# Kernel optimization log

Measured on AMD Instinct MI355X. Metric: run time of the kernel, lower is better.

## Reference

```python
import jax, jax.numpy as jnp
import numpy as np

N = 100000   # nodes per graph (50k users + 50k items)
E = 1600000  # edges per graph
D = 128      # feature / hidden dim
B = 100000   # train pairs per domain
NUM_USER = 50000
LAMBDA = 1.0


def setup_inputs() -> dict:
    key = jax.random.key(0)
    ks = jax.random.split(key, 24)
    s = 1.0 / np.sqrt(D)
    return {
        "feats_s": jax.random.normal(ks[0], (N, D), jnp.float32),
        "feats_t": jax.random.normal(ks[1], (N, D), jnp.float32),
        "W1": jax.random.normal(ks[2], (D, D), jnp.float32) * s,
        "b1": jnp.zeros((D,), jnp.float32),
        "W2": jax.random.normal(ks[3], (D, D), jnp.float32) * s,
        "b2": jnp.zeros((D,), jnp.float32),
        "cls_W": jax.random.normal(ks[4], (2 * D, 1), jnp.float32) * s,
        "cls_b": jnp.zeros((1,), jnp.float32),
        "du_W": jax.random.normal(ks[5], (D, 1), jnp.float32) * s,
        "du_b": jnp.zeros((1,), jnp.float32),
        "di_W": jax.random.normal(ks[6], (D, 1), jnp.float32) * s,
        "di_b": jnp.zeros((1,), jnp.float32),
        "edge_src_s": jax.random.randint(ks[7], (E,), 0, N, jnp.int32),
        "edge_dst_s": jax.random.randint(ks[8], (E,), 0, N, jnp.int32),
        "edge_src_t": jax.random.randint(ks[9], (E,), 0, N, jnp.int32),
        "edge_dst_t": jax.random.randint(ks[10], (E,), 0, N, jnp.int32),
        "user_s": jax.random.randint(ks[11], (B,), 0, NUM_USER, jnp.int32),
        "item_s": jax.random.randint(ks[12], (B,), 0, NUM_USER, jnp.int32),
        "labels_s": jax.random.randint(ks[13], (B,), 0, 2, jnp.int32),
        "user_t": jax.random.randint(ks[14], (B,), 0, NUM_USER, jnp.int32),
        "item_t": jax.random.randint(ks[15], (B,), 0, NUM_USER, jnp.int32),
        "labels_t": jax.random.randint(ks[16], (B,), 0, 2, jnp.int32),
        "num_user_ds": NUM_USER,
        "num_user_dt": NUM_USER,
    }


def _gcn_layer(x, W, b, src, dst, dinv):
    # PyG GCNConv: out[i] = sum_{j->i} dinv[j]*dinv[i] * (x @ W)[j] + b
    h = x @ W
    norm = (dinv[src] * dinv[dst])[:, None]
    return jax.ops.segment_sum(h[src] * norm, dst, num_segments=x.shape[0]) + b


def _encode(x, src, dst, W1, b1, W2, b2):
    n = x.shape[0]
    sl = jnp.arange(n, dtype=src.dtype)            # self loops
    src = jnp.concatenate([src, sl])
    dst = jnp.concatenate([dst, sl])
    deg = jax.ops.segment_sum(jnp.ones_like(dst, dtype=x.dtype), dst, num_segments=n)
    dinv = jax.lax.rsqrt(jnp.maximum(deg, 1.0))    # deg >= 1 due to self loops
    h = jax.nn.relu(_gcn_layer(x, W1, b1, src, dst, dinv))
    return _gcn_layer(h, W2, b2, src, dst, dinv)   # dropout is identity at eval


def _bce_from_logits(z, y):
    # mean BCE on sigmoid(z), numerically stable
    return jnp.mean(y * jax.nn.softplus(-z) + (1.0 - y) * jax.nn.softplus(z))


def reference(feats_s, feats_t, W1, b1, W2, b2, cls_W, cls_b, du_W, du_b, di_W, di_b,
              edge_src_s, edge_dst_s, edge_src_t, edge_dst_t,
              user_s, item_s, labels_s, user_t, item_t, labels_t,
              num_user_ds, num_user_dt):
    x_ds = _encode(feats_s, edge_src_s, edge_dst_s, W1, b1, W2, b2)
    x_dt = _encode(feats_t, edge_src_t, edge_dst_t, W1, b1, W2, b2)

    ufs = x_ds[user_s]
    ifs = x_ds[item_s + num_user_ds]
    uft = x_dt[user_t]
    ift = x_dt[item_t + num_user_dt]

    z_s = (jnp.concatenate([ufs, ifs], axis=1) @ cls_W).reshape(-1) + cls_b[0]
    z_t = (jnp.concatenate([uft, ift], axis=1) @ cls_W).reshape(-1) + cls_b[0]
    clf_loss = _bce_from_logits(z_s, labels_s.astype(jnp.float32)) + \
               _bce_from_logits(z_t, labels_t.astype(jnp.float32))

    cu_s = jax.nn.sigmoid((ufs @ du_W).reshape(-1) + du_b[0])
    cu_t = jax.nn.sigmoid((uft @ du_W).reshape(-1) + du_b[0])
    ci_s = jax.nn.sigmoid((ifs @ di_W).reshape(-1) + di_b[0])
    ci_t = jax.nn.sigmoid((ift @ di_W).reshape(-1) + di_b[0])
    domain_loss = jnp.abs(jnp.mean(cu_s) - jnp.mean(cu_t)) + \
                  jnp.abs(jnp.mean(ci_s) - jnp.mean(ci_t))

    return clf_loss + LAMBDA * domain_loss
```

## Files before the change

### kernel.cpp

```cpp
#include <hip/hip_runtime.h>

#define D 128
#define NB 512
#define BSLACK 4160
#define CHUNK 8

typedef __attribute__((ext_vector_type(8))) short bf16x8;
typedef __attribute__((ext_vector_type(4))) float f32x4;
typedef __attribute__((ext_vector_type(2))) float f32x2;
typedef __attribute__((ext_vector_type(4))) int i32x4;

static __device__ inline unsigned pack_bf16x2(float a, float b) {
    unsigned ua = __float_as_uint(a);
    unsigned ub = __float_as_uint(b);
    ua += 0x7fffu + ((ua >> 16) & 1u);
    ub += 0x7fffu + ((ub >> 16) & 1u);
    return (ua >> 16) | (ub & 0xffff0000u);
}

__global__ __launch_bounds__(256) void bh_k(const int* __restrict__ dst_s,
                                            const int* __restrict__ dst_t,
                                            int* __restrict__ bcnt, int E) {
    int d = blockIdx.y;
    const int* dst = d ? dst_t : dst_s;
    __shared__ int h[NB];
    for (int i = threadIdx.x; i < NB; i += 256) h[i] = 0;
    __syncthreads();
    int stride = gridDim.x * 256;
    for (int e = blockIdx.x * 256 + threadIdx.x; e < E; e += stride)
        atomicAdd(&h[dst[e] >> 8], 1);
    __syncthreads();
    for (int i = threadIdx.x; i < NB; i += 256)
        if (h[i]) atomicAdd(&bcnt[d * NB + i], h[i]);
}

__global__ __launch_bounds__(1024) void scanB_k(const int* __restrict__ bcnt,
                                                int* __restrict__ bbase,
                                                int* __restrict__ cursor) {
    __shared__ int sh[1024];
    int t = threadIdx.x;
    int v = bcnt[t];
    sh[t] = v;
    __syncthreads();
    for (int o = 1; o < 1024; o <<= 1) {
        int x = (t >= o) ? sh[t - o] : 0;
        __syncthreads();
        sh[t] += x;
        __syncthreads();
    }
    int ex = sh[t] - v;
    bbase[t] = ex; cursor[t] = ex;
    if (t == 1023) bbase[1024] = sh[1023];
}

__global__ __launch_bounds__(256) void bin_k(const int* __restrict__ src_s,
                                             const int* __restrict__ dst_s,
                                             const int* __restrict__ src_t,
                                             const int* __restrict__ dst_t,
                                             int* __restrict__ cursor,
                                             unsigned* __restrict__ pairs, int E) {
    int d = blockIdx.y;
    const int* src = d ? src_t : src_s;
    const int* dst = d ? dst_t : dst_s;
    int* cur = cursor + d * NB;
    __shared__ int h[NB];
    __shared__ int gb[NB];
    int t0 = blockIdx.x * 2048;
    if (t0 >= E) return;
    for (int i = threadIdx.x; i < NB; i += 256) h[i] = 0;
    __syncthreads();
    int rank[8]; unsigned pk[8]; short bk[8];
    #pragma unroll
    for (int j = 0; j < 8; ++j) {
        int e = t0 + j * 256 + threadIdx.x;
        if (e < E) {
            int dd = dst[e], s = src[e];
            bk[j] = (short)(dd >> 8);
            pk[j] = (unsigned)s | ((unsigned)(dd & 255) << 24);
            rank[j] = atomicAdd(&h[dd >> 8], 1);
        } else bk[j] = -1;
    }
    __syncthreads();
    for (int i = threadIdx.x; i < NB; i += 256)
        gb[i] = h[i] ? atomicAdd(&cur[i], h[i]) : 0;
    __syncthreads();
    #pragma unroll
    for (int j = 0; j < 8; ++j)
        if (bk[j] >= 0) pairs[gb[bk[j]] + rank[j]] = pk[j];
}

__global__ __launch_bounds__(256) void csrb_k(const unsigned* __restrict__ pairs,
                                              const int* __restrict__ bbase,
                                              int2* __restrict__ nspan,
                                              float* __restrict__ dinv,
                                              int* __restrict__ csr, int N) {
    int d = blockIdx.y, bx = blockIdx.x, t = threadIdx.x;
    int g = d * NB + bx;
    int e0 = bbase[g], e1 = bbase[g + 1];
    int cbase = ((e0 + 15) & ~15) + g * BSLACK;
    float* dv = dinv + (size_t)d * (N + 1);
    int2* ns = nspan + (size_t)d * N;
    __shared__ int lh[256];
    __shared__ int lex[256];
    __shared__ int lc[256];
    lh[t] = 0; lc[t] = 0;
    __syncthreads();
    for (int e = e0 + t; e < e1; e += 256)
        atomicAdd(&lh[pairs[e] >> 24], 1);
    __syncthreads();
    int node = (bx << 8) + t;
    bool valid = node < N;
    int deg = lh[t];
    int pdeg = valid ? (((deg + 16) >> 4) << 4) : 0;
    lex[t] = pdeg;
    __syncthreads();
    for (int o = 1; o < 256; o <<= 1) {
        int x = (t >= o) ? lex[t - o] : 0;
        __syncthreads();
        lex[t] += x;
        __syncthreads();
    }
    int start = cbase + lex[t] - pdeg;
    if (valid) {
        ns[node] = make_int2(start, start + pdeg);
        dv[node] = rsqrtf((float)(deg + 1));
    }
    lex[t] = start;
    __syncthreads();
    for (int e = e0 + t; e < e1; e += 256) {
        unsigned p = pairs[e];
        int dn = p >> 24;
        int rank = atomicAdd(&lc[dn], 1);
        csr[lex[dn] + rank] = (int)(p & 0xffffffu);
    }
    __syncthreads();
    if (valid) {
        int b = lex[t];
        csr[b + deg] = node;
        for (int k = deg + 1; k < pdeg; ++k) csr[b + k] = N;
    }
    if (t == 255) {
        int bend = start + pdeg;
        #pragma unroll
        for (int i = 0; i < 16; ++i) csr[bend + i] = N;
    }
    if (bx == 0 && t == 0) dv[N] = 0.f;
}

__global__ __launch_bounds__(256) void packW_k(const float* __restrict__ W1,
                                               const float* __restrict__ W2,
                                               unsigned short* __restrict__ wp1,
                                               unsigned short* __restrict__ wp2) {
    const float* W = blockIdx.x ? W2 : W1;
    unsigned short* wp = blockIdx.x ? wp2 : wp1;
    for (int idx = threadIdx.x; idx < 2048; idx += 256) {
        int f = idx >> 6, lane = idx & 63;
        int t = f >> 2, c = f & 3;
        int q = lane >> 4, nn = lane & 15;
        #pragma unroll
        for (int j = 0; j < 8; ++j) {
            unsigned u = __float_as_uint(W[(c * 32 + q * 8 + j) * 128 + t * 16 + nn]);
            u += 0x7fffu + ((u >> 16) & 1u);
            wp[idx * 8 + j] = (unsigned short)(u >> 16);
        }
    }
}

__global__ __launch_bounds__(256) void gemm_mfma(const void* __restrict__ xs,
                                                 const void* __restrict__ xt,
                                                 const unsigned short* __restrict__ wp,
                                                 unsigned* __restrict__ hb,
                                                 const float* __restrict__ dinv,
                                                 int N, int in_bf16) {
    int d = blockIdx.y;
    const void* xin = d ? xt : xs;
    unsigned* out = hb + (size_t)d * (N + 1) * 32;
    const float* dv = dinv + (size_t)d * (N + 1);
    __shared__ float cs[64 * 132];
    int tid = threadIdx.x;
    int wave = tid >> 6, lane = tid & 63;
    int quad = lane >> 4, nn = lane & 15;
    long long blockbase = (long long)blockIdx.x * 64;
    long long ar = blockbase + wave * 16 + nn;
    if (ar > N - 1) ar = N - 1;

    bf16x8 a[4];
    if (in_bf16) {
        const uint4* xr = (const uint4*)((const unsigned short*)xin + ar * 128);
        #pragma unroll
        for (int c = 0; c < 4; ++c) {
            union { uint4 u; bf16x8 v; } cv;
            cv.u = xr[c * 4 + quad];
            a[c] = cv.v;
        }
    } else {
        const float4* xr = (const float4*)((const float*)xin + ar * 128);
        #pragma unroll
        for (int c = 0; c < 4; ++c) {
            float4 lo = xr[c * 8 + quad * 2];
            float4 hi = xr[c * 8 + quad * 2 + 1];
            union { bf16x8 v; unsigned u[4]; } au;
            au.u[0] = pack_bf16x2(lo.x, lo.y);
            au.u[1] = pack_bf16x2(lo.z, lo.w);
            au.u[2] = pack_bf16x2(hi.x, hi.y);
            au.u[3] = pack_bf16x2(hi.z, hi.w);
            a[c] = au.v;
        }
    }

    f32x4 acc[8];
    #pragma unroll
    for (int t = 0; t < 8; ++t) acc[t] = (f32x4){0.f, 0.f, 0.f, 0.f};
    const bf16x8* wf = (const bf16x8*)wp;
    #pragma unroll
    for (int t = 0; t < 8; ++t) {
        #pragma unroll
        for (int c = 0; c < 4; ++c) {
            bf16x8 b = wf[(t * 4 + c) * 64 + lane];
            acc[t] = __builtin_amdgcn_mfma_f32_16x16x32_bf16(a[c], b, acc[t], 0, 0, 0);
        }
    }

    #pragma unroll
    for (int t = 0; t < 8; ++t) {
        #pragma unroll
        for (int r = 0; r < 4; ++r)
            cs[(wave * 16 + quad * 4 + r) * 132 + t * 16 + nn] = acc[t][r];
    }
    __syncthreads();

    #pragma unroll
    for (int i = 0; i < 8; ++i) {
        int idx = tid + i * 256;
        int r = idx >> 5, c4 = idx & 31;
        long long row = blockbase + r;
        if (row <= N) {
            float s = dv[row];
            const float4 v = *(const float4*)&cs[r * 132 + c4 * 4];
            int pk = __builtin_amdgcn_cvt_pk_fp8_f32(v.x * s, v.y * s, 0, false);
            pk = __builtin_amdgcn_cvt_pk_fp8_f32(v.z * s, v.w * s, pk, true);
            out[row * 32 + c4] = (unsigned)pk;
        }
    }
}

#define NTLD(p) __builtin_nontemporal_load((const i32x4*)(p))

#define AGG_GATHER(u, q0, q1)                                                \
        u[0] = hsl[(unsigned)q0.x << 5];                                     \
        u[1] = hsl[(unsigned)q0.y << 5];                                     \
        u[2] = hsl[(unsigned)q0.z << 5];                                     \
        u[3] = hsl[(unsigned)q0.w << 5];                                     \
        u[4] = hsl[(unsigned)q1.x << 5];                                     \
        u[5] = hsl[(unsigned)q1.y << 5];                                     \
        u[6] = hsl[(unsigned)q1.z << 5];                                     \
        u[7] = hsl[(unsigned)q1.w << 5];

#define AGG_CONSUME(u)                                                       \
        { f32x2 lo, hi;                                                      \
          lo = __builtin_amdgcn_cvt_pk_f32_fp8((int)u[0], false);            \
          hi = __builtin_amdgcn_cvt_pk_f32_fp8((int)u[0], true);             \
          s01 += lo; s23 += hi;                                              \
          lo = __builtin_amdgcn_cvt_pk_f32_fp8((int)u[1], false);            \
          hi = __builtin_amdgcn_cvt_pk_f32_fp8((int)u[1], true);             \
          s01 += lo; s23 += hi;                                              \
          lo = __builtin_amdgcn_cvt_pk_f32_fp8((int)u[2], false);            \
          hi = __builtin_amdgcn_cvt_pk_f32_fp8((int)u[2], true);             \
          s01 += lo; s23 += hi;                                              \
          lo = __builtin_amdgcn_cvt_pk_f32_fp8((int)u[3], false);            \
          hi = __builtin_amdgcn_cvt_pk_f32_fp8((int)u[3], true);             \
          s01 += lo; s23 += hi;                                              \
          lo = __builtin_amdgcn_cvt_pk_f32_fp8((int)u[4], false);            \
          hi = __builtin_amdgcn_cvt_pk_f32_fp8((int)u[4], true);             \
          s01 += lo; s23 += hi;                                              \
          lo = __builtin_amdgcn_cvt_pk_f32_fp8((int)u[5], false);            \
          hi = __builtin_amdgcn_cvt_pk_f32_fp8((int)u[5], true);             \
          s01 += lo; s23 += hi;                                              \
          lo = __builtin_amdgcn_cvt_pk_f32_fp8((int)u[6], false);            \
          hi = __builtin_amdgcn_cvt_pk_f32_fp8((int)u[6], true);             \
          s01 += lo; s23 += hi;                                              \
          lo = __builtin_amdgcn_cvt_pk_f32_fp8((int)u[7], false);            \
          hi = __builtin_amdgcn_cvt_pk_f32_fp8((int)u[7], true);             \
          s01 += lo; s23 += hi; }

__global__ __launch_bounds__(256) void agg1_k(const unsigned* __restrict__ hb,
                                              const float* __restrict__ dinv,
                                              const int2* __restrict__ nspan,
                                              const int* __restrict__ csr,
                                              const float* __restrict__ bias,
                                              uint2* __restrict__ abuf, int N) {
    int d = blockIdx.y;
    const unsigned* hs = hb + (size_t)d * (N + 1) * 32;
    const float* dv = dinv + (size_t)d * (N + 1);
    const int2* ns = nspan + (size_t)d * N;
    uint2* out = abuf + (size_t)d * N * 32;
    int wave = threadIdx.x >> 6, lane = threadIdx.x & 63;
    int node0 = (blockIdx.x * 4 + wave) * CHUNK;
    if (node0 >= N) return;
    int cnt = min(CHUNK, N - node0);
    int half = lane >> 5, li = lane & 31;
    int lc = lane & (CHUNK - 1);
    int2 myns = make_int2(0, 0);
    float mydv = 0.f;
    if (lc < cnt) { myns = ns[node0 + lc]; mydv = dv[node0 + lc]; }
    float4 b4 = ((const float4*)bias)[li];
    const unsigned* hsl = hs + li;
    const int* cp = csr + 8 * half;

    f32x2 s01 = (f32x2){0.f, 0.f};
    f32x2 s23 = (f32x2){0.f, 0.f};

    auto finalize = [&](int k) {
        float a0 = s01[0], a1 = s01[1], a2 = s23[0], a3 = s23[1];
        a0 += __shfl_xor(a0, 32);
        a1 += __shfl_xor(a1, 32);
        a2 += __shfl_xor(a2, 32);
        a3 += __shfl_xor(a3, 32);
        float dik = __shfl(mydv, k);
        float o0 = fmaxf(fmaf(dik, a0, b4.x), 0.f);
        float o1 = fmaxf(fmaf(dik, a1, b4.y), 0.f);
        float o2 = fmaxf(fmaf(dik, a2, b4.z), 0.f);
        float o3 = fmaxf(fmaf(dik, a3, b4.w), 0.f);
        if (half == 0)
            out[(size_t)(node0 + k) * 32 + li] =
                make_uint2(pack_bf16x2(o0, o1), pack_bf16x2(o2, o3));
    };

    int k = 0;
    int e = __shfl(myns.x, 0);
    int end = __shfl(myns.y, 0);
    i32x4 c0 = NTLD(cp + e), c1 = NTLD(cp + e + 4);
    unsigned uA[8], uB[8];
    AGG_GATHER(uA, c0, c1)
    c0 = NTLD(cp + e + 16); c1 = NTLD(cp + e + 20);
    for (;;) {
        int en = e + 16;
        AGG_GATHER(uB, c0, c1)
        c0 = NTLD(cp + en + 16); c1 = NTLD(cp + en + 20);
        AGG_CONSUME(uA)
        if (en >= end) {
            finalize(k);
            if (++k >= cnt) break;
            end = __shfl(myns.y, k);
            s01 = (f32x2){0.f, 0.f};
            s23 = (f32x2){0.f, 0.f};
        }
        e = en;
        en = e + 16;
        AGG_GATHER(uA, c0, c1)
        c0 = NTLD(cp + en + 16); c1 = NTLD(cp + en + 20);
        AGG_CONSUME(uB)
        if (en >= end) {
            finalize(k);
            if (++k >= cnt) break;
            end = __shfl(myns.y, k);
            s01 = (f32x2){0.f, 0.f};
            s23 = (f32x2){0.f, 0.f};
        }
        e = en;
    }
}

__global__ __launch_bounds__(256) void agg2_k(const unsigned* __restrict__ hb,
                                              const float* __restrict__ dinv,
                                              const int2* __restrict__ nspan,
                                              const int* __restrict__ csr,
                                              const float* __restrict__ bias,
                                              const float* __restrict__ clsW,
                                              const float* __restrict__ duW,
                                              const float* __restrict__ diW,
                                              const int* __restrict__ nus,
                                              const int* __restrict__ nut,
                                              float2* __restrict__ nodeDots, int N) {
    int d = blockIdx.y;
    const unsigned* hs = hb + (size_t)d * (N + 1) * 32;
    const float* dv = dinv + (size_t)d * (N + 1);
    const int2* ns = nspan + (size_t)d * N;
    float2* nd = nodeDots + (size_t)d * N;
    int nu = d ? nut[0] : nus[0];
    int wave = threadIdx.x >> 6, lane = threadIdx.x & 63;
    int node0 = (blockIdx.x * 4 + wave) * CHUNK;
    if (node0 >= N) return;
    int cnt = min(CHUNK, N - node0);
    int half = lane >> 5, li = lane & 31;
    int lc = lane & (CHUNK - 1);
    int2 myns = make_int2(0, 0);
    float mydv = 0.f;
    if (lc < cnt) { myns = ns[node0 + lc]; mydv = dv[node0 + lc]; }
    float4 b4 = ((const float4*)bias)[li];
    float4 wA0 = ((const float4*)clsW)[li];
    float4 wA1 = ((const float4*)clsW)[32 + li];
    float4 wB0 = ((const float4*)duW)[li];
    float4 wB1 = ((const float4*)diW)[li];
    const unsigned* hsl = hs + li;
    const int* cp = csr + 8 * half;

    f32x2 s01 = (f32x2){0.f, 0.f};
    f32x2 s23 = (f32x2){0.f, 0.f};

    auto finalize = [&](int k) {
        float a0 = s01[0], a1 = s01[1], a2 = s23[0], a3 = s23[1];
        a0 += __shfl_xor(a0, 32);
        a1 += __shfl_xor(a1, 32);
        a2 += __shfl_xor(a2, 32);
        a3 += __shfl_xor(a3, 32);
        float dik = __shfl(mydv, k);
        float o0 = fmaf(dik, a0, b4.x);
        float o1 = fmaf(dik, a1, b4.y);
        float o2 = fmaf(dik, a2, b4.z);
        float o3 = fmaf(dik, a3, b4.w);
        int nodek = node0 + k;
        int sel = (nodek >= nu) ? 1 : 0;
        float4 wA = sel ? wA1 : wA0;
        float4 wB = sel ? wB1 : wB0;
        float p = o0 * wA.x + o1 * wA.y + o2 * wA.z + o3 * wA.w;
        float q = o0 * wB.x + o1 * wB.y + o2 * wB.z + o3 * wB.w;
        #pragma unroll
        for (int o = 16; o > 0; o >>= 1) {
            p += __shfl_xor(p, o);
            q += __shfl_xor(q, o);
        }
        if (lane == 0) nd[nodek] = make_float2(p, q);
    };

    int k = 0;
    int e = __shfl(myns.x, 0);
    int end = __shfl(myns.y, 0);
    i32x4 c0 = NTLD(cp + e), c1 = NTLD(cp + e + 4);
    unsigned uA[8], uB[8];
    AGG_GATHER(uA, c0, c1)
    c0 = NTLD(cp + e + 16); c1 = NTLD(cp + e + 20);
    for (;;) {
        int en = e + 16;
        AGG_GATHER(uB, c0, c1)
        c0 = NTLD(cp + en + 16); c1 = NTLD(cp + en + 20);
        AGG_CONSUME(uA)
        if (en >= end) {
            finalize(k);
            if (++k >= cnt) break;
            end = __shfl(myns.y, k);
            s01 = (f32x2){0.f, 0.f};
            s23 = (f32x2){0.f, 0.f};
        }
        e = en;
        en = e + 16;
        AGG_GATHER(uA, c0, c1)
        c0 = NTLD(cp + en + 16); c1 = NTLD(cp + en + 20);
        AGG_CONSUME(uB)
        if (en >= end) {
            finalize(k);
            if (++k >= cnt) break;
            end = __shfl(myns.y, k);
            s01 = (f32x2){0.f, 0.f};
            s23 = (f32x2){0.f, 0.f};
        }
        e = en;
    }
}

__global__ __launch_bounds__(256) void loss_k(const float2* __restrict__ nodeDots,
                                              const int* __restrict__ us, const int* __restrict__ is_,
                                              const int* __restrict__ ls,
                                              const int* __restrict__ ut, const int* __restrict__ it,
                                              const int* __restrict__ lt,
                                              const float* __restrict__ clsb,
                                              const float* __restrict__ dub,
                                              const float* __restrict__ dib,
                                              const int* __restrict__ nus,
                                              const int* __restrict__ nut,
                                              float* __restrict__ accum, int Bn, int N) {
    int d = blockIdx.y;
    const float2* nd = nodeDots + (size_t)d * N;
    const int* users = d ? ut : us;
    const int* items = d ? it : is_;
    const int* labels = d ? lt : ls;
    int nu = d ? nut[0] : nus[0];
    float* acc = accum + 3 * d;
    int k = blockIdx.x * 256 + threadIdx.x;
    float bce = 0.f, cu = 0.f, ci = 0.f;
    if (k < Bn) {
        int u = users[k];
        int t = items[k] + nu;
        float2 ud = nd[u];
        float2 id = nd[t];
        float z = ud.x + id.x + clsb[0];
        float y = (float)labels[k];
        float sp = fmaxf(z, 0.f) + log1pf(expf(-fabsf(z)));
        bce = sp - y * z;
        cu = 1.f / (1.f + expf(-(ud.y + dub[0])));
        ci = 1.f / (1.f + expf(-(id.y + dib[0])));
    }
    #pragma unroll
    for (int o = 32; o > 0; o >>= 1) {
        bce += __shfl_xor(bce, o);
        cu += __shfl_xor(cu, o);
        ci += __shfl_xor(ci, o);
    }
    __shared__ float sh[12];
    int lane = threadIdx.x & 63, wave = threadIdx.x >> 6;
    if (lane == 0) { sh[wave * 3 + 0] = bce; sh[wave * 3 + 1] = cu; sh[wave * 3 + 2] = ci; }
    __syncthreads();
    if (threadIdx.x < 3) {
        float v = sh[threadIdx.x] + sh[3 + threadIdx.x] + sh[6 + threadIdx.x] + sh[9 + threadIdx.x];
        atomicAdd(&acc[threadIdx.x], v);
    }
}

__global__ void finalize_k(const float* __restrict__ accum, float* __restrict__ out, float invB) {
    if (threadIdx.x == 0 && blockIdx.x == 0) {
        float clf = (accum[0] + accum[3]) * invB;
        float dom = fabsf((accum[1] - accum[4]) * invB) + fabsf((accum[2] - accum[5]) * invB);
        out[0] = clf + dom;
    }
}

extern "C" void kernel_launch(void* const* d_in, const int* in_sizes, int n_in,
                              void* d_out, int out_size, void* d_ws, size_t ws_size,
                              hipStream_t stream) {
    const float* feats_s = (const float*)d_in[0];
    const float* feats_t = (const float*)d_in[1];
    const float* W1   = (const float*)d_in[2];
    const float* b1   = (const float*)d_in[3];
    const float* W2   = (const float*)d_in[4];
    const float* b2   = (const float*)d_in[5];
    const float* clsW = (const float*)d_in[6];
    const float* clsb = (const float*)d_in[7];
    const float* duW  = (const float*)d_in[8];
    const float* dub  = (const float*)d_in[9];
    const float* diW  = (const float*)d_in[10];
    const float* dib  = (const float*)d_in[11];

    int N = in_sizes[0] / D;
    int E = in_sizes[12];
    int B = in_sizes[16];
    int nb = (N + 255) >> 8;

    char* ws = (char*)d_ws;
    size_t off = 0;
    auto alloc = [&](size_t bytes) -> void* {
        void* p = ws + off;
        off += (bytes + 255) & ~(size_t)255;
        return p;
    };
    int*      bcnt   = (int*)  alloc(2 * NB * 4);
    int*      bbase  = (int*)  alloc((2 * NB + 1) * 4);
    int*      cursor = (int*)  alloc(2 * NB * 4);
    float*    dinv   = (float*)alloc((size_t)2 * (N + 1) * 4);
    int2*     nspan  = (int2*) alloc((size_t)2 * N * 8);
    unsigned* pairs  = (unsigned*)alloc((size_t)2 * E * 4);
    int*      csr    = (int*)  alloc(((size_t)2 * E + 2 * NB * BSLACK + 256) * 4);
    unsigned* hbuf8  = (unsigned*)alloc((size_t)2 * (N + 1) * 128);
    unsigned* abuf   = (unsigned*)alloc((size_t)2 * N * 256);
    float2*   nodeDots = (float2*)alloc((size_t)2 * N * 8);
    unsigned short* wp1 = (unsigned short*)alloc(16384 * 2);
    unsigned short* wp2 = (unsigned short*)alloc(16384 * 2);
    float*    accum  = (float*)alloc(128);

    hipMemsetAsync(accum, 0, 6 * sizeof(float), stream);
    hipMemsetAsync(bcnt, 0, 2 * NB * 4, stream);

    const int* esrc_s = (const int*)d_in[12];
    const int* edst_s = (const int*)d_in[13];
    const int* esrc_t = (const int*)d_in[14];
    const int* edst_t = (const int*)d_in[15];
    const int* user_s = (const int*)d_in[16];
    const int* item_s = (const int*)d_in[17];
    const int* lab_s  = (const int*)d_in[18];
    const int* user_t = (const int*)d_in[19];
    const int* item_t = (const int*)d_in[20];
    const int* lab_t  = (const int*)d_in[21];
    const int* nup_s  = (const int*)d_in[22];
    const int* nup_t  = (const int*)d_in[23];

    packW_k<<<2, 256, 0, stream>>>(W1, W2, wp1, wp2);

    bh_k<<<dim3(512, 2), 256, 0, stream>>>(edst_s, edst_t, bcnt, E);
    scanB_k<<<1, 1024, 0, stream>>>(bcnt, bbase, cursor);
    bin_k<<<dim3((E + 2047) / 2048, 2), 256, 0, stream>>>(esrc_s, edst_s, esrc_t, edst_t,
                                                          cursor, pairs, E);
    csrb_k<<<dim3(nb, 2), 256, 0, stream>>>(pairs, bbase, nspan, dinv, csr, N);

    int ngb = (N + 64) / 64;
    int nchunk = (N + CHUNK - 1) / CHUNK;
    gemm_mfma<<<dim3(ngb, 2), 256, 0, stream>>>(feats_s, feats_t, wp1, hbuf8, dinv, N, 0);
    agg1_k<<<dim3((nchunk + 3) / 4, 2), 256, 0, stream>>>(hbuf8, dinv, nspan, csr, b1,
                                                          (uint2*)abuf, N);
    gemm_mfma<<<dim3(ngb, 2), 256, 0, stream>>>(abuf, abuf + (size_t)N * 64, wp2,
                                                hbuf8, dinv, N, 1);
    agg2_k<<<dim3((nchunk + 3) / 4, 2), 256, 0, stream>>>(hbuf8, dinv, nspan, csr, b2,
                                                          clsW, duW, diW, nup_s, nup_t,
                                                          nodeDots, N);
    loss_k<<<dim3((B + 255) / 256, 2), 256, 0, stream>>>(nodeDots,
                                                         user_s, item_s, lab_s,
                                                         user_t, item_t, lab_t,
                                                         clsb, dub, dib, nup_s, nup_t,
                                                         accum, B, N);
    finalize_k<<<1, 64, 0, stream>>>(accum, (float*)d_out, 1.0f / (float)B);
}
```

Measured before the change: 484.2 us.

## Deepen gather pipeline in aggregation kernels to three stages and shrink histogram grid

```diff
diff --git a/kernel.cpp b/kernel.cpp
--- a/kernel.cpp
+++ b/kernel.cpp
@@ -141,8 +141,7 @@
     }
     if (t == 255) {
         int bend = start + pdeg;
-        #pragma unroll
-        for (int i = 0; i < 16; ++i) csr[bend + i] = N;
+        for (int i = 0; i < 48; ++i) csr[bend + i] = N;
     }
     if (bx == 0 && t == 0) dv[N] = 0.f;
 }
@@ -247,14 +246,14 @@
 #define NTLD(p) __builtin_nontemporal_load((const i32x4*)(p))
 
 #define AGG_GATHER(u, q0, q1)                                                \
-        u[0] = hsl[(unsigned)q0.x << 5];                                     \
-        u[1] = hsl[(unsigned)q0.y << 5];                                     \
-        u[2] = hsl[(unsigned)q0.z << 5];                                     \
-        u[3] = hsl[(unsigned)q0.w << 5];                                     \
-        u[4] = hsl[(unsigned)q1.x << 5];                                     \
-        u[5] = hsl[(unsigned)q1.y << 5];                                     \
-        u[6] = hsl[(unsigned)q1.z << 5];                                     \
-        u[7] = hsl[(unsigned)q1.w << 5];
+        u[0] = hsl[((unsigned)(q0).x) << 5];                                 \
+        u[1] = hsl[((unsigned)(q0).y) << 5];                                 \
+        u[2] = hsl[((unsigned)(q0).z) << 5];                                 \
+        u[3] = hsl[((unsigned)(q0).w) << 5];                                 \
+        u[4] = hsl[((unsigned)(q1).x) << 5];                                 \
+        u[5] = hsl[((unsigned)(q1).y) << 5];                                 \
+        u[6] = hsl[((unsigned)(q1).z) << 5];                                 \
+        u[7] = hsl[((unsigned)(q1).w) << 5];
 
 #define AGG_CONSUME(u)                                                       \
         { f32x2 lo, hi;                                                      \
@@ -283,17 +282,52 @@
           hi = __builtin_amdgcn_cvt_pk_f32_fp8((int)u[7], true);             \
           s01 += lo; s23 += hi; }
 
-__global__ __launch_bounds__(256) void agg1_k(const unsigned* __restrict__ hb,
-                                              const float* __restrict__ dinv,
-                                              const int2* __restrict__ nspan,
-                                              const int* __restrict__ csr,
-                                              const float* __restrict__ bias,
-                                              uint2* __restrict__ abuf, int N) {
+#define BOUND                                                                \
+        if (en >= end) {                                                     \
+            finalize(k);                                                     \
+            if (++k >= cnt) break;                                           \
+            end = __shfl(myns.y, k);                                         \
+            s01 = (f32x2){0.f, 0.f};                                         \
+            s23 = (f32x2){0.f, 0.f};                                         \
+        }                                                                    \
+        e = en;
+
+#define AGG_PIPE_LOOP                                                        \
+    i32x4 a0 = NTLD(cp + e), a1 = NTLD(cp + e + 4);                          \
+    i32x4 b0 = NTLD(cp + e + 16), b1 = NTLD(cp + e + 20);                    \
+    i32x4 t0 = NTLD(cp + e + 32), t1 = NTLD(cp + e + 36);                    \
+    unsigned uA[8], uB[8], uC[8];                                            \
+    AGG_GATHER(uA, a0, a1)                                                   \
+    AGG_GATHER(uB, b0, b1)                                                   \
+    for (;;) {                                                               \
+        int en = e + 16;                                                     \
+        AGG_GATHER(uC, t0, t1)                                               \
+        a0 = NTLD(cp + e + 48); a1 = NTLD(cp + e + 52);                      \
+        AGG_CONSUME(uA)                                                      \
+        BOUND                                                                \
+        en = e + 16;                                                         \
+        AGG_GATHER(uA, a0, a1)                                               \
+        b0 = NTLD(cp + e + 48); b1 = NTLD(cp + e + 52);                      \
+        AGG_CONSUME(uB)                                                      \
+        BOUND                                                                \
+        en = e + 16;                                                         \
+        AGG_GATHER(uB, b0, b1)                                               \
+        t0 = NTLD(cp + e + 48); t1 = NTLD(cp + e + 52);                      \
+        AGG_CONSUME(uC)                                                      \
+        BOUND                                                                \
+    }
+
+__global__ __launch_bounds__(256, 4) void agg1_k(const unsigned* __restrict__ hb,
+                                                 const float* __restrict__ dinv,
+                                                 const int2* __restrict__ nspan,
+                                                 const int* __restrict__ csr,
+                                                 const float* __restrict__ bias,
+                                                 uint2* __restrict__ out, int N) {
     int d = blockIdx.y;
     const unsigned* hs = hb + (size_t)d * (N + 1) * 32;
     const float* dv = dinv + (size_t)d * (N + 1);
     const int2* ns = nspan + (size_t)d * N;
-    uint2* out = abuf + (size_t)d * N * 32;
+    uint2* outp = out + (size_t)d * N * 32;
     int wave = threadIdx.x >> 6, lane = threadIdx.x & 63;
     int node0 = (blockIdx.x * 4 + wave) * CHUNK;
     if (node0 >= N) return;
@@ -310,68 +344,39 @@
     f32x2 s01 = (f32x2){0.f, 0.f};
     f32x2 s23 = (f32x2){0.f, 0.f};
 
-    auto finalize = [&](int k) {
+    auto finalize = [&](int kk) {
         float a0 = s01[0], a1 = s01[1], a2 = s23[0], a3 = s23[1];
         a0 += __shfl_xor(a0, 32);
         a1 += __shfl_xor(a1, 32);
         a2 += __shfl_xor(a2, 32);
         a3 += __shfl_xor(a3, 32);
-        float dik = __shfl(mydv, k);
+        float dik = __shfl(mydv, kk);
         float o0 = fmaxf(fmaf(dik, a0, b4.x), 0.f);
         float o1 = fmaxf(fmaf(dik, a1, b4.y), 0.f);
         float o2 = fmaxf(fmaf(dik, a2, b4.z), 0.f);
         float o3 = fmaxf(fmaf(dik, a3, b4.w), 0.f);
         if (half == 0)
-            out[(size_t)(node0 + k) * 32 + li] =
+            outp[(size_t)(node0 + kk) * 32 + li] =
                 make_uint2(pack_bf16x2(o0, o1), pack_bf16x2(o2, o3));
     };
 
     int k = 0;
     int e = __shfl(myns.x, 0);
     int end = __shfl(myns.y, 0);
-    i32x4 c0 = NTLD(cp + e), c1 = NTLD(cp + e + 4);
-    unsigned uA[8], uB[8];
-    AGG_GATHER(uA, c0, c1)
-    c0 = NTLD(cp + e + 16); c1 = NTLD(cp + e + 20);
-    for (;;) {
-        int en = e + 16;
-        AGG_GATHER(uB, c0, c1)
-        c0 = NTLD(cp + en + 16); c1 = NTLD(cp + en + 20);
-        AGG_CONSUME(uA)
-        if (en >= end) {
-            finalize(k);
-            if (++k >= cnt) break;
-            end = __shfl(myns.y, k);
-            s01 = (f32x2){0.f, 0.f};
-            s23 = (f32x2){0.f, 0.f};
-        }
-        e = en;
-        en = e + 16;
-        AGG_GATHER(uA, c0, c1)
-        c0 = NTLD(cp + en + 16); c1 = NTLD(cp + en + 20);
-        AGG_CONSUME(uB)
-        if (en >= end) {
-            finalize(k);
-            if (++k >= cnt) break;
-            end = __shfl(myns.y, k);
-            s01 = (f32x2){0.f, 0.f};
-            s23 = (f32x2){0.f, 0.f};
-        }
-        e = en;
-    }
-}
-
-__global__ __launch_bounds__(256) void agg2_k(const unsigned* __restrict__ hb,
-                                              const float* __restrict__ dinv,
-                                              const int2* __restrict__ nspan,
-                                              const int* __restrict__ csr,
-                                              const float* __restrict__ bias,
-                                              const float* __restrict__ clsW,
-                                              const float* __restrict__ duW,
-                                              const float* __restrict__ diW,
-                                              const int* __restrict__ nus,
-                                              const int* __restrict__ nut,
-                                              float2* __restrict__ nodeDots, int N) {
+    AGG_PIPE_LOOP
+}
+
+__global__ __launch_bounds__(256, 4) void agg2_k(const unsigned* __restrict__ hb,
+                                                 const float* __restrict__ dinv,
+                                                 const int2* __restrict__ nspan,
+                                                 const int* __restrict__ csr,
+                                                 const float* __restrict__ bias,
+                                                 const float* __restrict__ clsW,
+                                                 const float* __restrict__ duW,
+                                                 const float* __restrict__ diW,
+                                                 const int* __restrict__ nus,
+                                                 const int* __restrict__ nut,
+                                                 float2* __restrict__ nodeDots, int N) {
     int d = blockIdx.y;
     const unsigned* hs = hb + (size_t)d * (N + 1) * 32;
     const float* dv = dinv + (size_t)d * (N + 1);
@@ -398,18 +403,18 @@
     f32x2 s01 = (f32x2){0.f, 0.f};
     f32x2 s23 = (f32x2){0.f, 0.f};
 
-    auto finalize = [&](int k) {
+    auto finalize = [&](int kk) {
         float a0 = s01[0], a1 = s01[1], a2 = s23[0], a3 = s23[1];
         a0 += __shfl_xor(a0, 32);
         a1 += __shfl_xor(a1, 32);
         a2 += __shfl_xor(a2, 32);
         a3 += __shfl_xor(a3, 32);
-        float dik = __shfl(mydv, k);
+        float dik = __shfl(mydv, kk);
         float o0 = fmaf(dik, a0, b4.x);
         float o1 = fmaf(dik, a1, b4.y);
         float o2 = fmaf(dik, a2, b4.z);
         float o3 = fmaf(dik, a3, b4.w);
-        int nodek = node0 + k;
+        int nodek = node0 + kk;
         int sel = (nodek >= nu) ? 1 : 0;
         float4 wA = sel ? wA1 : wA0;
         float4 wB = sel ? wB1 : wB0;
@@ -426,36 +431,7 @@
     int k = 0;
     int e = __shfl(myns.x, 0);
     int end = __shfl(myns.y, 0);
-    i32x4 c0 = NTLD(cp + e), c1 = NTLD(cp + e + 4);
-    unsigned uA[8], uB[8];
-    AGG_GATHER(uA, c0, c1)
-    c0 = NTLD(cp + e + 16); c1 = NTLD(cp + e + 20);
-    for (;;) {
-        int en = e + 16;
-        AGG_GATHER(uB, c0, c1)
-        c0 = NTLD(cp + en + 16); c1 = NTLD(cp + en + 20);
-        AGG_CONSUME(uA)
-        if (en >= end) {
-            finalize(k);
-            if (++k >= cnt) break;
-            end = __shfl(myns.y, k);
-            s01 = (f32x2){0.f, 0.f};
-            s23 = (f32x2){0.f, 0.f};
-        }
-        e = en;
-        en = e + 16;
-        AGG_GATHER(uA, c0, c1)
-        c0 = NTLD(cp + en + 16); c1 = NTLD(cp + en + 20);
-        AGG_CONSUME(uB)
-        if (en >= end) {
-            finalize(k);
-            if (++k >= cnt) break;
-            end = __shfl(myns.y, k);
-            s01 = (f32x2){0.f, 0.f};
-            s23 = (f32x2){0.f, 0.f};
-        }
-        e = en;
-    }
+    AGG_PIPE_LOOP
 }
 
 __global__ __launch_bounds__(256) void loss_k(const float2* __restrict__ nodeDots,
@@ -574,7 +550,7 @@
 
     packW_k<<<2, 256, 0, stream>>>(W1, W2, wp1, wp2);
 
-    bh_k<<<dim3(512, 2), 256, 0, stream>>>(edst_s, edst_t, bcnt, E);
+    bh_k<<<dim3(64, 2), 256, 0, stream>>>(edst_s, edst_t, bcnt, E);
     scanB_k<<<1, 1024, 0, stream>>>(bcnt, bbase, cursor);
     bin_k<<<dim3((E + 2047) / 2048, 2), 256, 0, stream>>>(esrc_s, edst_s, esrc_t, edst_t,
                                                           cursor, pairs, E);
```

Result: slower. 516.5 us (+6.7%).
